# Kernel optimization log

Measured on AMD Instinct MI355X. Metric: run time of the kernel, lower is better.

The kernel has to match this reference:

```python
import jax, jax.numpy as jnp
import numpy as np

L = 5   # local window size (l)
R = 2   # upsample factor (r)


def setup_inputs() -> dict:
    key = jax.random.key(0)
    k0, k1, k2 = jax.random.split(key, 3)
    B, C, H, W, OUT = 4, 128, 64, 64, 128
    x = jax.random.normal(k0, (B, C, H, W), jnp.float32)
    # conv1: in_channels -> l^2, 3x3, pad 1 (with bias, as nn.Conv2d default)
    w1 = jax.random.normal(k1, (L * L, C, 3, 3), jnp.float32) * 0.05
    b1 = jnp.zeros((L * L,), jnp.float32)
    # conv2: 4*in_channels -> out_channels, 1x1 (stored as [out, 4C])
    w2 = jax.random.normal(k2, (OUT, 4 * C), jnp.float32) * 0.05
    b2 = jnp.zeros((OUT,), jnp.float32)
    return {"x": x, "w1": w1, "b1": b1, "w2": w2, "b2": b2}


def _upsample2_nearest(t):
    # nearest-neighbor x2 upsample on NCHW
    return jnp.repeat(jnp.repeat(t, R, axis=2), R, axis=3)


def reference(x, w1, b1, w2, b2):
    B, C, H, W = x.shape
    # conv1 (3x3, SAME) -> [B, L^2, H, W]
    k = jax.lax.conv_general_dilated(
        x, w1, window_strides=(1, 1), padding='SAME',
        dimension_numbers=('NCHW', 'OIHW', 'NCHW')) + b1[None, :, None, None]
    # nearest x2 upsample then softmax over the L^2 channel dim
    k = _upsample2_nearest(k)                 # [B, L^2, 2H, 2W]
    k = jax.nn.softmax(k, axis=1)
    # non-overlapping RxR block extraction (unfold size=R, step=R twice)
    # -> [B, L^2, H, W, R^2], last-dim order (row-offset, col-offset)
    k = k.reshape(B, L * L, H, R, W, R).transpose(0, 1, 2, 4, 3, 5)
    k = k.reshape(B, L * L, H, W, R * R)
    # overlapping LxL window extraction of the input (unfold size=L, step=1)
    pad = L // 2
    xp = jnp.pad(x, ((0, 0), (0, 0), (pad, pad), (pad, pad)))
    wins = jnp.stack(
        [xp[:, :, i:i + H, j:j + W] for i in range(L) for j in range(L)],
        axis=-1)                               # [B, C, H, W, L^2]
    # per-pixel matmul: [C, L^2] @ [L^2, R^2] -> [B, H, W, C, R^2]
    out = jnp.einsum('bchwk,bkhwr->bhwcr', wins, k)
    # flatten (C, R^2) -> 4C (C-major, matching torch reshape), back to NCHW
    out = out.reshape(B, H, W, C * R * R).transpose(0, 3, 1, 2)
    out = _upsample2_nearest(out)              # [B, 4C, 2H, 2W]
    # conv2: 1x1 -> out_channels
    out = jnp.einsum('bchw,oc->bohw', out, w2) + b2[None, :, None, None]
    return out
```

## Files before the change

kernel.cpp:

```cpp
#include <hip/hip_runtime.h>
#include <math.h>

#define BB   4
#define CC   128
#define HH   64
#define WW   64
#define OUTC 128
#define KK   25
#define PXB  16
#define SJ   20

typedef __attribute__((ext_vector_type(8))) short short8;
typedef _Float16 half8  __attribute__((ext_vector_type(8)));
typedef __fp16   fp16x2 __attribute__((ext_vector_type(2)));
typedef __attribute__((ext_vector_type(4))) float floatx4;

__device__ __forceinline__ unsigned short f32_to_bf16(float v) {
    unsigned int u = __float_as_uint(v);
    u += 0x7fffu + ((u >> 16) & 1u);
    return (unsigned short)(u >> 16);
}

__global__ void prep_kernel(const float* __restrict__ w2,
                            const float* __restrict__ w1,
                            unsigned short* __restrict__ w2o,
                            unsigned short* __restrict__ w1f) {
    int i = blockIdx.x * 256 + threadIdx.x;
    if (i < 16384) {
        int o = i >> 7, c = i & 127;
        const float* p = w2 + o * (4 * CC) + c * 4;
        w2o[o * CC + c] = f32_to_bf16(p[0] + p[1] + p[2] + p[3]);
    } else if (i < 16384 + 36864) {
        int f = i - 16384;
        int i8   = f & 7;
        int lane = (f >> 3) & 63;
        int ks   = (f >> 9) & 3;
        int mt   = (f >> 11) & 1;
        int dydx = f >> 12;
        int kk = mt * 16 + (lane & 15);
        int c  = ks * 32 + (lane >> 4) * 8 + i8;
        float v = (kk < KK) ? w1[(size_t)(kk * CC + c) * 9 + dydx] : 0.f;
        _Float16 hv = (_Float16)v;
        w1f[f] = *(unsigned short*)&hv;
    }
}

__global__ __launch_bounds__(128, 2) void fused_kernel(
        const float* __restrict__ x,
        const unsigned short* __restrict__ w1f,
        const unsigned short* __restrict__ w2o,
        const float* __restrict__ b1,
        const float* __restrict__ b2,
        float* __restrict__ out) {
    __shared__ _Float16 xs[3 * SJ * 128];
    __shared__ float pk[KK * PXB];
    unsigned short* sKT = (unsigned short*)xs;

    int bid0 = blockIdx.x;
    int bid  = (bid0 & 7) * 128 + (bid0 >> 3);
    int wq = bid & 3;
    int h  = (bid >> 2) & 63;
    int b  = bid >> 8;
    int t  = threadIdx.x;
    int lane = t & 63;
    int wv = t >> 6;

    const float* xb = x + (size_t)b * CC * (HH * WW);

    {
        int jj = lane & 15, cp = lane >> 4;
        int j  = jj + 2;
        int swz = (j & 15) << 3;
        float mr_[3]; int yo_[3];
        #pragma unroll
        for (int r = 0; r < 3; ++r) {
            int y = h - 1 + r;
            mr_[r] = (y >= 0 && y < HH) ? 1.f : 0.f;
            yo_[r] = min(max(y, 0), HH - 1) * WW;
        }
        float v0s[24], v1s[24];
        #pragma unroll
        for (int ci = 0; ci < 8; ++ci) {
            int c = wv * 64 + ci * 8 + cp * 2;
            const float* xc0 = xb + (size_t)c * (HH * WW) + wq * 16 + jj;
            const float* xc1 = xc0 + HH * WW;
            #pragma unroll
            for (int r = 0; r < 3; ++r) {
                v0s[ci * 3 + r] = xc0[yo_[r]];
                v1s[ci * 3 + r] = xc1[yo_[r]];
            }
        }
        #pragma unroll
        for (int ci = 0; ci < 8; ++ci) {
            int c  = wv * 64 + ci * 8 + cp * 2;
            int cs = c ^ swz;
            #pragma unroll
            for (int r = 0; r < 3; ++r) {
                fp16x2 p = __builtin_amdgcn_cvt_pkrtz(
                    v0s[ci * 3 + r] * mr_[r], v1s[ci * 3 + r] * mr_[r]);
                *(fp16x2*)&xs[(r * SJ + j) * 128 + cs] = p;
            }
        }
        float hv[12], hm[12];
        #pragma unroll
        for (int k = 0; k < 12; ++k) {
            int i  = t + k * 128;
            int jh = i & 3;
            int c  = (i >> 2) & 127;
            int r  = i >> 9;
            int j2 = (jh < 2) ? jh : 16 + jh;
            int xcol = wq * 16 + j2 - 2;
            int y = h - 1 + r;
            bool inb = (xcol >= 0 && xcol < WW && y >= 0 && y < HH);
            int yc  = min(max(y, 0), HH - 1);
            int xc2 = min(max(xcol, 0), WW - 1);
            hv[k] = xb[(size_t)c * (HH * WW) + yc * WW + xc2];
            hm[k] = inb ? 1.f : 0.f;
        }
        #pragma unroll
        for (int k = 0; k < 12; ++k) {
            int i  = t + k * 128;
            int jh = i & 3;
            int c  = (i >> 2) & 127;
            int r  = i >> 9;
            int j2 = (jh < 2) ? jh : 16 + jh;
            xs[(r * SJ + j2) * 128 + (c ^ ((j2 & 15) << 3))] =
                (_Float16)(hv[k] * hm[k]);
        }
    }
    __syncthreads();

    int fpx = lane & 15, quad = lane >> 4;
    int mt = wv;
    floatx4 acc0 = {0.f, 0.f, 0.f, 0.f};
    floatx4 acc1 = {0.f, 0.f, 0.f, 0.f};
    __builtin_amdgcn_s_setprio(1);
    #pragma unroll
    for (int dydx = 0; dydx < 9; ++dydx) {
        int r   = dydx / 3;
        int dxm = dydx - 3 * r;
        int j   = fpx + dxm + 1;
        int rowbase = (r * SJ + j) * 128;
        int swz = (j & 15) << 3;
        const unsigned short* whb = w1f + (dydx * 2 + mt) * 2048 + lane * 8;
        floatx4& accr = (dydx & 1) ? acc1 : acc0;
        #pragma unroll
        for (int ks = 0; ks < 4; ++ks) {
            int cb = (ks * 32 + quad * 8) ^ swz;
            half8 A = *(const half8*)(whb + ks * 512);
            half8 B = *(const half8*)&xs[rowbase + cb];
            accr = __builtin_amdgcn_mfma_f32_16x16x32_f16(A, B, accr, 0, 0, 0);
        }
    }
    __builtin_amdgcn_s_setprio(0);
    floatx4 accs = acc0 + acc1;
    #pragma unroll
    for (int reg = 0; reg < 4; ++reg) {
        int kk = mt * 16 + quad * 4 + reg;
        if (kk < KK) pk[kk * PXB + fpx] = accs[reg] + b1[kk];
    }
    __syncthreads();

    int pp2 = t & 7, cw = t >> 3;

    int colg = wq * 16 + 2 * pp2 - 2;
    int coff[3]; float cmask[3];
    #pragma unroll
    for (int jx = 0; jx < 3; ++jx) {
        int cg = colg + 2 * jx;
        cmask[jx] = (cg >= 0 && cg <= WW - 2) ? 1.f : 0.f;
        coff[jx]  = min(max(cg, 0), WW - 2);
    }
    int yoff[5]; float msk[15];
    #pragma unroll
    for (int di = 0; di < 5; ++di) {
        int y = h + di - 2;
        float rm = (y >= 0 && y < HH) ? 1.f : 0.f;
        yoff[di] = min(max(y, 0), HH - 1) * WW;
        #pragma unroll
        for (int jx = 0; jx < 3; ++jx) msk[di * 3 + jx] = rm * cmask[jx];
    }

    float2 lg[KK];
    #pragma unroll
    for (int k = 0; k < KK; ++k) lg[k] = *(const float2*)&pk[k * PXB + 2 * pp2];
    float m0 = -1e30f, m1 = -1e30f;
    #pragma unroll
    for (int k = 0; k < KK; ++k) { m0 = fmaxf(m0, lg[k].x); m1 = fmaxf(m1, lg[k].y); }
    float s0 = 0.f, s1 = 0.f;
    #pragma unroll
    for (int k = 0; k < KK; ++k) {
        lg[k].x = __expf(lg[k].x - m0); s0 += lg[k].x;
        lg[k].y = __expf(lg[k].y - m1); s1 += lg[k].y;
    }
    float i0 = 1.f / s0, i1 = 1.f / s1;
    #pragma unroll
    for (int k = 0; k < KK; ++k) { lg[k].x *= i0; lg[k].y *= i1; }
    #pragma unroll
    for (int di = 0; di < 5; ++di)
        #pragma unroll
        for (int dj = 0; dj < 5; ++dj) {
            lg[di * 5 + dj].x *= msk[di * 3 + (dj >> 1)];
            lg[di * 5 + dj].y *= msk[di * 3 + ((dj + 1) >> 1)];
        }

#define LOADC(BUF, I8) do {                                            \
    int c_ = (I8) * 16 + cw;                                           \
    const float* xc_ = xb + (size_t)c_ * (HH * WW);                    \
    _Pragma("unroll")                                                  \
    for (int di = 0; di < 5; ++di)                                     \
        _Pragma("unroll")                                              \
        for (int jx = 0; jx < 3; ++jx)                                 \
            BUF[di * 3 + jx] = *(const float2*)(xc_ + yoff[di] + coff[jx]); \
} while (0)

#define COMPST(BUF, I8) do {                                           \
    float t0 = 0.f, t1 = 0.f;                                          \
    _Pragma("unroll")                                                  \
    for (int di = 0; di < 5; ++di) {                                   \
        float2 x01 = BUF[di * 3 + 0];                                  \
        float2 x23 = BUF[di * 3 + 1];                                  \
        float2 x45 = BUF[di * 3 + 2];                                  \
        t0 += lg[di*5+0].x * x01.x + lg[di*5+1].x * x01.y              \
            + lg[di*5+2].x * x23.x + lg[di*5+3].x * x23.y              \
            + lg[di*5+4].x * x45.x;                                    \
        t1 += lg[di*5+0].y * x01.y + lg[di*5+1].y * x23.x              \
            + lg[di*5+2].y * x23.y + lg[di*5+3].y * x45.x              \
            + lg[di*5+4].y * x45.y;                                    \
    }                                                                  \
    int cs_ = (I8) * 16 + cw;                                          \
    sKT[(2 * pp2) * 136 + cs_]     = f32_to_bf16(t0);                  \
    sKT[(2 * pp2 + 1) * 136 + cs_] = f32_to_bf16(t1);                  \
} while (0)

    {
        float2 bufA[15], bufB[15];
        LOADC(bufA, 0);
        LOADC(bufB, 1);
        COMPST(bufA, 0); LOADC(bufA, 2);
        COMPST(bufB, 1); LOADC(bufB, 3);
        COMPST(bufA, 2); LOADC(bufA, 4);
        COMPST(bufB, 3); LOADC(bufB, 5);
        COMPST(bufA, 4); LOADC(bufA, 6);
        COMPST(bufB, 5); LOADC(bufB, 7);
        COMPST(bufA, 6);
        COMPST(bufB, 7);
    }
    __syncthreads();

    floatx4 am[4] = {{0.f,0.f,0.f,0.f},{0.f,0.f,0.f,0.f},
                     {0.f,0.f,0.f,0.f},{0.f,0.f,0.f,0.f}};
    __builtin_amdgcn_s_setprio(1);
    #pragma unroll
    for (int ks = 0; ks < 4; ++ks) {
        short8 bf = *(const short8*)&sKT[fpx * 136 + ks*32 + quad*8];
        #pragma unroll
        for (int mt2 = 0; mt2 < 4; ++mt2) {
            short8 af = *(const short8*)&w2o[(size_t)(64*wv + 16*mt2 + fpx) * CC
                                             + ks*32 + quad*8];
            am[mt2] = __builtin_amdgcn_mfma_f32_16x16x32_bf16(af, bf, am[mt2], 0, 0, 0);
        }
    }
    __builtin_amdgcn_s_setprio(0);

    float* ob = out + (size_t)b * OUTC * (4 * HH * WW);
    int y0 = 2 * h;
    int pxo = wq * 16 + fpx;
    #pragma unroll
    for (int mt2 = 0; mt2 < 4; ++mt2) {
        #pragma unroll
        for (int reg = 0; reg < 4; ++reg) {
            int o = 64*wv + 16*mt2 + quad*4 + reg;
            float v = am[mt2][reg] + b2[o];
            float2 v2 = make_float2(v, v);
            float* r0p = ob + ((size_t)o * (2*HH) + y0) * (2*WW) + 2*pxo;
            *(float2*)(r0p)        = v2;
            *(float2*)(r0p + 2*WW) = v2;
        }
    }
}

extern "C" void kernel_launch(void* const* d_in, const int* in_sizes, int n_in,
                              void* d_out, int out_size, void* d_ws, size_t ws_size,
                              hipStream_t stream) {
    const float* x  = (const float*)d_in[0];
    const float* w1 = (const float*)d_in[1];
    const float* b1 = (const float*)d_in[2];
    const float* w2 = (const float*)d_in[3];
    const float* b2 = (const float*)d_in[4];
    float* out = (float*)d_out;

    unsigned short* w2o = (unsigned short*)d_ws;
    unsigned short* w1f = w2o + (size_t)OUTC * CC;

    prep_kernel<<<(16384 + 36864 + 255) / 256, 256, 0, stream>>>(w2, w1, w2o, w1f);
    fused_kernel<<<BB * HH * 4, 128, 0, stream>>>(x, w1f, w2o, b1, b2, out);
}
```

Before: 95.02 us.

## Double block size to 256 threads and split work across four waves

Raises the fused kernel from two to four waves per block. The conv1 MFMA reduction is split across K halves and combined through two shared logit buffers. The window pass and the conv2 output tiles are split so each wave handles half as many channels. The aim is more latency hiding and parallelism per tile, at the cost of an extra shared buffer, an added partial-sum step and higher register and occupancy pressure under the 256-thread launch bound.

```diff
diff --git a/kernel.cpp b/kernel.cpp
--- a/kernel.cpp
+++ b/kernel.cpp
@@ -45,7 +45,7 @@
     }
 }
 
-__global__ __launch_bounds__(128, 2) void fused_kernel(
+__global__ __launch_bounds__(256, 2) void fused_kernel(
         const float* __restrict__ x,
         const unsigned short* __restrict__ w1f,
         const unsigned short* __restrict__ w2o,
@@ -53,7 +53,8 @@
         const float* __restrict__ b2,
         float* __restrict__ out) {
     __shared__ _Float16 xs[3 * SJ * 128];
-    __shared__ float pk[KK * PXB];
+    __shared__ float pk0[KK * PXB];
+    __shared__ float pk1[KK * PXB];
     unsigned short* sKT = (unsigned short*)xs;
 
     int bid0 = blockIdx.x;
@@ -78,10 +79,10 @@
             mr_[r] = (y >= 0 && y < HH) ? 1.f : 0.f;
             yo_[r] = min(max(y, 0), HH - 1) * WW;
         }
-        float v0s[24], v1s[24];
-        #pragma unroll
-        for (int ci = 0; ci < 8; ++ci) {
-            int c = wv * 64 + ci * 8 + cp * 2;
+        float v0s[12], v1s[12];
+        #pragma unroll
+        for (int ci = 0; ci < 4; ++ci) {
+            int c = wv * 32 + ci * 8 + cp * 2;
             const float* xc0 = xb + (size_t)c * (HH * WW) + wq * 16 + jj;
             const float* xc1 = xc0 + HH * WW;
             #pragma unroll
@@ -91,8 +92,8 @@
             }
         }
         #pragma unroll
-        for (int ci = 0; ci < 8; ++ci) {
-            int c  = wv * 64 + ci * 8 + cp * 2;
+        for (int ci = 0; ci < 4; ++ci) {
+            int c  = wv * 32 + ci * 8 + cp * 2;
             int cs = c ^ swz;
             #pragma unroll
             for (int r = 0; r < 3; ++r) {
@@ -101,10 +102,10 @@
                 *(fp16x2*)&xs[(r * SJ + j) * 128 + cs] = p;
             }
         }
-        float hv[12], hm[12];
-        #pragma unroll
-        for (int k = 0; k < 12; ++k) {
-            int i  = t + k * 128;
+        float hv[6], hm[6];
+        #pragma unroll
+        for (int k = 0; k < 6; ++k) {
+            int i  = t + k * 256;
             int jh = i & 3;
             int c  = (i >> 2) & 127;
             int r  = i >> 9;
@@ -118,8 +119,8 @@
             hm[k] = inb ? 1.f : 0.f;
         }
         #pragma unroll
-        for (int k = 0; k < 12; ++k) {
-            int i  = t + k * 128;
+        for (int k = 0; k < 6; ++k) {
+            int i  = t + k * 256;
             int jh = i & 3;
             int c  = (i >> 2) & 127;
             int r  = i >> 9;
@@ -131,9 +132,8 @@
     __syncthreads();
 
     int fpx = lane & 15, quad = lane >> 4;
-    int mt = wv;
-    floatx4 acc0 = {0.f, 0.f, 0.f, 0.f};
-    floatx4 acc1 = {0.f, 0.f, 0.f, 0.f};
+    int mt = wv & 1, kh = wv >> 1;
+    floatx4 acc = {0.f, 0.f, 0.f, 0.f};
     __builtin_amdgcn_s_setprio(1);
     #pragma unroll
     for (int dydx = 0; dydx < 9; ++dydx) {
@@ -143,21 +143,24 @@
         int rowbase = (r * SJ + j) * 128;
         int swz = (j & 15) << 3;
         const unsigned short* whb = w1f + (dydx * 2 + mt) * 2048 + lane * 8;
-        floatx4& accr = (dydx & 1) ? acc1 : acc0;
-        #pragma unroll
-        for (int ks = 0; ks < 4; ++ks) {
+        #pragma unroll
+        for (int kq = 0; kq < 2; ++kq) {
+            int ks = kh * 2 + kq;
             int cb = (ks * 32 + quad * 8) ^ swz;
             half8 A = *(const half8*)(whb + ks * 512);
             half8 B = *(const half8*)&xs[rowbase + cb];
-            accr = __builtin_amdgcn_mfma_f32_16x16x32_f16(A, B, accr, 0, 0, 0);
+            acc = __builtin_amdgcn_mfma_f32_16x16x32_f16(A, B, acc, 0, 0, 0);
         }
     }
     __builtin_amdgcn_s_setprio(0);
-    floatx4 accs = acc0 + acc1;
-    #pragma unroll
-    for (int reg = 0; reg < 4; ++reg) {
-        int kk = mt * 16 + quad * 4 + reg;
-        if (kk < KK) pk[kk * PXB + fpx] = accs[reg] + b1[kk];
+    {
+        float* pkh = kh ? pk1 : pk0;
+        #pragma unroll
+        for (int reg = 0; reg < 4; ++reg) {
+            int kk = mt * 16 + quad * 4 + reg;
+            if (kk < KK)
+                pkh[kk * PXB + fpx] = acc[reg] + (kh ? 0.f : b1[kk]);
+        }
     }
     __syncthreads();
 
@@ -183,7 +186,11 @@
 
     float2 lg[KK];
     #pragma unroll
-    for (int k = 0; k < KK; ++k) lg[k] = *(const float2*)&pk[k * PXB + 2 * pp2];
+    for (int k = 0; k < KK; ++k) {
+        float2 a = *(const float2*)&pk0[k * PXB + 2 * pp2];
+        float2 c2 = *(const float2*)&pk1[k * PXB + 2 * pp2];
+        lg[k] = make_float2(a.x + c2.x, a.y + c2.y);
+    }
     float m0 = -1e30f, m1 = -1e30f;
     #pragma unroll
     for (int k = 0; k < KK; ++k) { m0 = fmaxf(m0, lg[k].x); m1 = fmaxf(m1, lg[k].y); }
@@ -204,8 +211,8 @@
             lg[di * 5 + dj].y *= msk[di * 3 + ((dj + 1) >> 1)];
         }
 
-#define LOADC(BUF, I8) do {                                            \
-    int c_ = (I8) * 16 + cw;                                           \
+#define LOADC(BUF, I4) do {                                            \
+    int c_ = (I4) * 32 + cw;                                           \
     const float* xc_ = xb + (size_t)c_ * (HH * WW);                    \
     _Pragma("unroll")                                                  \
     for (int di = 0; di < 5; ++di)                                     \
@@ -214,7 +221,7 @@
             BUF[di * 3 + jx] = *(const float2*)(xc_ + yoff[di] + coff[jx]); \
 } while (0)
 
-#define COMPST(BUF, I8) do {                                           \
+#define COMPST(BUF, I4) do {                                           \
     float t0 = 0.f, t1 = 0.f;                                          \
     _Pragma("unroll")                                                  \
     for (int di = 0; di < 5; ++di) {                                   \
@@ -228,7 +235,7 @@
             + lg[di*5+2].y * x23.y + lg[di*5+3].y * x45.x              \
             + lg[di*5+4].y * x45.y;                                    \
     }                                                                  \
-    int cs_ = (I8) * 16 + cw;                                          \
+    int cs_ = (I4) * 32 + cw;                                          \
     sKT[(2 * pp2) * 136 + cs_]     = f32_to_bf16(t0);                  \
     sKT[(2 * pp2 + 1) * 136 + cs_] = f32_to_bf16(t1);                  \
 } while (0)
@@ -239,27 +246,20 @@
         LOADC(bufB, 1);
         COMPST(bufA, 0); LOADC(bufA, 2);
         COMPST(bufB, 1); LOADC(bufB, 3);
-        COMPST(bufA, 2); LOADC(bufA, 4);
-        COMPST(bufB, 3); LOADC(bufB, 5);
-        COMPST(bufA, 4); LOADC(bufA, 6);
-        COMPST(bufB, 5); LOADC(bufB, 7);
-        COMPST(bufA, 6);
-        COMPST(bufB, 7);
+        COMPST(bufA, 2);
+        COMPST(bufB, 3);
     }
     __syncthreads();
 
-    floatx4 am[4] = {{0.f,0.f,0.f,0.f},{0.f,0.f,0.f,0.f},
-                     {0.f,0.f,0.f,0.f},{0.f,0.f,0.f,0.f}};
+    floatx4 am[2] = {{0.f,0.f,0.f,0.f},{0.f,0.f,0.f,0.f}};
     __builtin_amdgcn_s_setprio(1);
     #pragma unroll
     for (int ks = 0; ks < 4; ++ks) {
-        short8 bf = *(const short8*)&sKT[fpx * 136 + ks*32 + quad*8];
-        #pragma unroll
-        for (int mt2 = 0; mt2 < 4; ++mt2) {
-            short8 af = *(const short8*)&w2o[(size_t)(64*wv + 16*mt2 + fpx) * CC
-                                             + ks*32 + quad*8];
-            am[mt2] = __builtin_amdgcn_mfma_f32_16x16x32_bf16(af, bf, am[mt2], 0, 0, 0);
-        }
+        short8 bf  = *(const short8*)&sKT[fpx * 136 + ks*32 + quad*8];
+        short8 af0 = *(const short8*)&w2o[(size_t)(32*wv      + fpx) * CC + ks*32 + quad*8];
+        short8 af1 = *(const short8*)&w2o[(size_t)(32*wv + 16 + fpx) * CC + ks*32 + quad*8];
+        am[0] = __builtin_amdgcn_mfma_f32_16x16x32_bf16(af0, bf, am[0], 0, 0, 0);
+        am[1] = __builtin_amdgcn_mfma_f32_16x16x32_bf16(af1, bf, am[1], 0, 0, 0);
     }
     __builtin_amdgcn_s_setprio(0);
 
@@ -267,10 +267,10 @@
     int y0 = 2 * h;
     int pxo = wq * 16 + fpx;
     #pragma unroll
-    for (int mt2 = 0; mt2 < 4; ++mt2) {
+    for (int mt2 = 0; mt2 < 2; ++mt2) {
         #pragma unroll
         for (int reg = 0; reg < 4; ++reg) {
-            int o = 64*wv + 16*mt2 + quad*4 + reg;
+            int o = 32*wv + 16*mt2 + quad*4 + reg;
             float v = am[mt2][reg] + b2[o];
             float2 v2 = make_float2(v, v);
             float* r0p = ob + ((size_t)o * (2*HH) + y0) * (2*WW) + 2*pxo;
@@ -294,5 +294,5 @@
     unsigned short* w1f = w2o + (size_t)OUTC * CC;
 
     prep_kernel<<<(16384 + 36864 + 255) / 256, 256, 0, stream>>>(w2, w1, w2o, w1f);
-    fused_kernel<<<BB * HH * 4, 128, 0, stream>>>(x, w1f, w2o, b1, b2, out);
-}
+    fused_kernel<<<BB * HH * 4, 256, 0, stream>>>(x, w1f, w2o, b1, b2, out);
+}
```

Result: no change. 94.72 us (-0.3%).
